# Performance work log

Hardware: AMD Instinct MI355X
Metric: run time of the kernel (lower is better)

The kernel has to match this reference:

```python
import jax, jax.numpy as jnp
import numpy as np

B, T, D = 2048, 200, 256

def setup_inputs() -> dict:
    key = jax.random.key(0)
    k1, k2, k3, k4, k5 = jax.random.split(key, 5)
    query = jax.random.normal(k1, (B, 1, D), dtype=jnp.float32)
    user_behavior = jax.random.normal(k2, (B, T, D), dtype=jnp.float32)
    mask = jax.random.bernoulli(k3, 0.5, (B, T))
    # nn.Linear weights: linear1 (2D -> D), linear2 (D -> 1), no bias
    W1 = jax.random.normal(k4, (D, 2 * D), dtype=jnp.float32) * (1.0 / np.sqrt(2 * D))
    W2 = jax.random.normal(k5, (1, D), dtype=jnp.float32) * (1.0 / np.sqrt(D))
    return {"query": query, "user_behavior": user_behavior, "mask": mask, "W1": W1, "W2": W2}

def reference(query, user_behavior, mask, W1, W2):
    T_ = user_behavior.shape[1]
    queries = jnp.broadcast_to(query, (query.shape[0], T_, query.shape[2]))  # [B,T,D]
    attn_in = jnp.concatenate([queries, user_behavior], axis=-1)  # [B,T,2D]
    h = jnp.tanh(jnp.einsum('btk,dk->btd', attn_in, W1))          # [B,T,D]
    score = jnp.einsum('btd,od->bot', h, W2)                       # [B,1,T] (transpose(1,2) of [B,T,1])
    # masked_fill with 0 BEFORE softmax, as in the original module
    score = jnp.where(mask[:, None, :], jnp.zeros((), score.dtype), score)
    attn = jax.nn.softmax(score, axis=-1)                          # [B,1,T]
    out = jnp.matmul(attn, user_behavior)                          # [B,1,D]
    return jnp.squeeze(out)                                        # [B,D]
```

## Files before the change

### kernel.cpp

```cpp
#include <hip/hip_runtime.h>
#include <hip/hip_bf16.h>

typedef __bf16 bf16_t;
typedef __bf16 bf16x8 __attribute__((ext_vector_type(8)));
typedef float  f32x4  __attribute__((ext_vector_type(4)));

#define T_LEN 200
#define D_DIM 256
#define NTILE 13
#define NB    2

__device__ __forceinline__ float fast_tanh(float x) {
    float e = __expf(2.0f * x);
    return 1.0f - 2.0f / (e + 1.0f);
}

__global__ __launch_bounds__(256) void qpart_kernel(
    const float* __restrict__ Q, const float* __restrict__ W1,
    float* __restrict__ Out)
{
    __shared__ float qs[8][256];
    const int tid = threadIdx.x;
    const int b0  = blockIdx.x * 8;
    for (int idx = tid; idx < 8 * 256; idx += 256)
        qs[idx >> 8][idx & 255] = Q[(size_t)(b0 + (idx >> 8)) * 256 + (idx & 255)];
    __syncthreads();
    float acc[8];
    #pragma unroll
    for (int i = 0; i < 8; ++i) acc[i] = 0.f;
    const f32x4* Wv = (const f32x4*)(W1 + (size_t)tid * 512);
    #pragma unroll 4
    for (int k4 = 0; k4 < 64; ++k4) {
        f32x4 w = Wv[k4];
        #pragma unroll
        for (int bb = 0; bb < 8; ++bb) {
            f32x4 qv = *(const f32x4*)&qs[bb][k4 * 4];
            acc[bb] += qv[0]*w[0] + qv[1]*w[1] + qv[2]*w[2] + qv[3]*w[3];
        }
    }
    #pragma unroll
    for (int bb = 0; bb < 8; ++bb)
        Out[(size_t)(b0 + bb) * 256 + tid] = acc[bb];
}

__global__ __launch_bounds__(512, 4) void attn_main_kernel(
    const float* __restrict__ U,
    const int*   __restrict__ Mask,
    const float* __restrict__ W1,
    const float* __restrict__ W2,
    float* __restrict__ Out)
{
    __shared__ bf16_t ubt[3][16 * 256];
    __shared__ float score_lds[NTILE][16];
    __shared__ int   msk_lds[208];
    __shared__ float out_lds[4][256];
    __shared__ float l_lds[4];

    const int tid  = threadIdx.x;
    const int lane = tid & 63;
    const int wv   = tid >> 6;
    const int lr   = lane & 15;
    const int lg   = lane >> 4;

    bf16x8 bq[2][8];
    float  w2v[2];
    #pragma unroll
    for (int n = 0; n < 2; ++n) {
        const int d = wv * 32 + n * 16 + lr;
        const float* wrow = W1 + (size_t)d * 512 + 256;
        #pragma unroll
        for (int kk = 0; kk < 8; ++kk) {
            const float* s = wrow + kk * 32 + lg * 8;
            f32x4 lo = *(const f32x4*)s;
            f32x4 hi = *(const f32x4*)(s + 4);
            bf16x8 v;
            v[0]=(bf16_t)lo[0]; v[1]=(bf16_t)lo[1]; v[2]=(bf16_t)lo[2]; v[3]=(bf16_t)lo[3];
            v[4]=(bf16_t)hi[0]; v[5]=(bf16_t)hi[1]; v[6]=(bf16_t)hi[2]; v[7]=(bf16_t)hi[3];
            bq[n][kk] = v;
        }
        w2v[n] = W2[d];
    }

    const int srow = tid >> 5;
    const int scol = (tid & 31) * 8;
    const unsigned swoff = (unsigned)srow * 512
                         + (((unsigned)scol * 2) ^ (((unsigned)srow & 7) << 4));
    const int dp = tid & 127;
    const int jg = tid >> 7;

    for (int bb = 0; bb < NB; ++bb) {
        const int b = blockIdx.x * NB + bb;
        const float* Ub = U + (size_t)b * (T_LEN * D_DIM);

        float qp[2];
        #pragma unroll
        for (int n = 0; n < 2; ++n)
            qp[n] = Out[(size_t)b * 256 + wv * 32 + n * 16 + lr];

        for (int idx = tid; idx < NTILE * 16; idx += 512)
            ((float*)score_lds)[idx] = 0.f;
        if (tid < 208)
            msk_lds[tid] = (tid < T_LEN) ? Mask[(size_t)b * T_LEN + tid] : 1;

        float op0 = 0.f, op1 = 0.f, l_part = 0.f;

        {
            const float* src = Ub + (size_t)srow * 256 + scol;
            f32x4 g0 = *(const f32x4*)src;
            f32x4 g1 = *(const f32x4*)(src + 4);
            bf16x8 v;
            v[0]=(bf16_t)g0[0]; v[1]=(bf16_t)g0[1]; v[2]=(bf16_t)g0[2]; v[3]=(bf16_t)g0[3];
            v[4]=(bf16_t)g1[0]; v[5]=(bf16_t)g1[1]; v[6]=(bf16_t)g1[2]; v[7]=(bf16_t)g1[3];
            *(bf16x8*)((char*)&ubt[0][0] + swoff) = v;
        }
        __syncthreads();

        for (int it = 0; it < NTILE; ++it) {
            char* const bcur = (char*)&ubt[it % 3][0];
            char* const bnxt = (char*)&ubt[(it + 1) % 3][0];

            f32x4 g0 = {0.f,0.f,0.f,0.f}, g1 = {0.f,0.f,0.f,0.f};
            bool stage_w = false;
            if (it + 1 < NTILE) {
                const int t = (it + 1) * 16 + srow;
                if (t < T_LEN) {
                    const float* src = Ub + (size_t)t * 256 + scol;
                    g0 = *(const f32x4*)src;
                    g1 = *(const f32x4*)(src + 4);
                    stage_w = true;
                }
            }

            f32x4 acc0 = {0.f,0.f,0.f,0.f}, acc1 = {0.f,0.f,0.f,0.f};
            #pragma unroll
            for (int kk = 0; kk < 8; ++kk) {
                const unsigned kb   = (unsigned)(kk * 64 + lg * 16);
                const unsigned aoff = (unsigned)lr * 512
                                    + (kb ^ (((unsigned)lr & 7) << 4));
                bf16x8 a = *(const bf16x8*)(bcur + aoff);
                acc0 = __builtin_amdgcn_mfma_f32_16x16x32_bf16(a, bq[0][kk], acc0, 0, 0, 0);
                acc1 = __builtin_amdgcn_mfma_f32_16x16x32_bf16(a, bq[1][kk], acc1, 0, 0, 0);
            }

            if (stage_w) {
                bf16x8 v;
                v[0]=(bf16_t)g0[0]; v[1]=(bf16_t)g0[1]; v[2]=(bf16_t)g0[2]; v[3]=(bf16_t)g0[3];
                v[4]=(bf16_t)g1[0]; v[5]=(bf16_t)g1[1]; v[6]=(bf16_t)g1[2]; v[7]=(bf16_t)g1[3];
                *(bf16x8*)(bnxt + swoff) = v;
            }

            float sp[4];
            #pragma unroll
            for (int r = 0; r < 4; ++r) {
                float h0 = fast_tanh(acc0[r] + qp[0]);
                float h1 = fast_tanh(acc1[r] + qp[1]);
                sp[r] = h0 * w2v[0] + h1 * w2v[1];
            }
            #pragma unroll
            for (int r = 0; r < 4; ++r) {
                sp[r] += __shfl_xor(sp[r], 1);
                sp[r] += __shfl_xor(sp[r], 2);
                sp[r] += __shfl_xor(sp[r], 4);
                sp[r] += __shfl_xor(sp[r], 8);
            }
            if (lr == 0) {
                #pragma unroll
                for (int r = 0; r < 4; ++r)
                    atomicAdd(&score_lds[it][lg * 4 + r], sp[r]);
            }

            __syncthreads();

            #pragma unroll
            for (int jj = 0; jj < 4; ++jj) {
                const int j = jg * 4 + jj;
                const int t = it * 16 + j;
                const float s = score_lds[it][j];
                float p = 0.f;
                if (t < T_LEN)
                    p = msk_lds[t] ? 1.0f : __expf(s);
                l_part += p;
                const unsigned off = (unsigned)j * 512
                                   + (((unsigned)dp * 4) ^ (((unsigned)j & 7) << 4));
                const unsigned w = *(const unsigned*)(bcur + off);
                const float u0 = __builtin_bit_cast(float, w << 16);
                const float u1 = __builtin_bit_cast(float, w & 0xffff0000u);
                op0 += p * u0;
                op1 += p * u1;
            }
        }

        out_lds[jg][dp * 2]     = op0;
        out_lds[jg][dp * 2 + 1] = op1;
        if ((tid & 127) == 0) l_lds[jg] = l_part;
        __syncthreads();
        if (tid < 256) {
            const float l = l_lds[0] + l_lds[1] + l_lds[2] + l_lds[3];
            const float o = out_lds[0][tid] + out_lds[1][tid]
                          + out_lds[2][tid] + out_lds[3][tid];
            Out[(size_t)b * 256 + tid] = o / l;
        }
        __syncthreads();
    }
}

extern "C" void kernel_launch(void* const* d_in, const int* in_sizes, int n_in,
                              void* d_out, int out_size, void* d_ws, size_t ws_size,
                              hipStream_t stream)
{
    const float* Q  = (const float*)d_in[0];
    const float* U  = (const float*)d_in[1];
    const int*   Mk = (const int*)d_in[2];
    const float* W1 = (const float*)d_in[3];
    const float* W2 = (const float*)d_in[4];
    float* Out = (float*)d_out;
    const int B = in_sizes[0] / D_DIM;

    qpart_kernel<<<dim3(B / 8), dim3(256), 0, stream>>>(Q, W1, Out);
    attn_main_kernel<<<dim3(B / NB), dim3(512), 0, stream>>>(U, Mk, W1, W2, Out);
}
```

Baseline: 207.3 us.

## Use one batch row per block and do the weighted sum after scoring

Each block now handles a single batch row instead of two, which doubles the grid. The per-tile weighted sum over bf16 LDS tiles is removed. Scores are accumulated for all tiles first, then softmax weights are computed once into LDS, and a final pass re-reads U from global memory in fp32 to form the output. This shortens the per-tile critical path and gives fp32 accuracy in the output sum, at the cost of a second read of each U row (likely served from L2) and a larger grid that reloads W1 fragments per row.

```diff
diff --git a/kernel.cpp b/kernel.cpp
--- a/kernel.cpp
+++ b/kernel.cpp
@@ -8,7 +8,6 @@
 #define T_LEN 200
 #define D_DIM 256
 #define NTILE 13
-#define NB    2
 
 __device__ __forceinline__ float fast_tanh(float x) {
     float e = __expf(2.0f * x);
@@ -51,16 +50,17 @@
     float* __restrict__ Out)
 {
     __shared__ bf16_t ubt[3][16 * 256];
-    __shared__ float score_lds[NTILE][16];
-    __shared__ int   msk_lds[208];
+    __shared__ float score_lds[208];
+    __shared__ float p_lds[208];
     __shared__ float out_lds[4][256];
-    __shared__ float l_lds[4];
+    __shared__ float l_lds;
 
     const int tid  = threadIdx.x;
     const int lane = tid & 63;
     const int wv   = tid >> 6;
     const int lr   = lane & 15;
     const int lg   = lane >> 4;
+    const int b    = blockIdx.x;
 
     bf16x8 bq[2][8];
     float  w2v[2];
@@ -81,126 +81,126 @@
         w2v[n] = W2[d];
     }
 
+    const float* Ub = U + (size_t)b * (T_LEN * D_DIM);
+
+    float qp[2];
+    #pragma unroll
+    for (int n = 0; n < 2; ++n)
+        qp[n] = Out[(size_t)b * 256 + wv * 32 + n * 16 + lr];
+
+    if (tid < 208) score_lds[tid] = 0.f;
+    if (tid == 0)  l_lds = 0.f;
+
     const int srow = tid >> 5;
     const int scol = (tid & 31) * 8;
     const unsigned swoff = (unsigned)srow * 512
                          + (((unsigned)scol * 2) ^ (((unsigned)srow & 7) << 4));
-    const int dp = tid & 127;
-    const int jg = tid >> 7;
-
-    for (int bb = 0; bb < NB; ++bb) {
-        const int b = blockIdx.x * NB + bb;
-        const float* Ub = U + (size_t)b * (T_LEN * D_DIM);
-
-        float qp[2];
-        #pragma unroll
-        for (int n = 0; n < 2; ++n)
-            qp[n] = Out[(size_t)b * 256 + wv * 32 + n * 16 + lr];
-
-        for (int idx = tid; idx < NTILE * 16; idx += 512)
-            ((float*)score_lds)[idx] = 0.f;
-        if (tid < 208)
-            msk_lds[tid] = (tid < T_LEN) ? Mask[(size_t)b * T_LEN + tid] : 1;
-
-        float op0 = 0.f, op1 = 0.f, l_part = 0.f;
-
-        {
-            const float* src = Ub + (size_t)srow * 256 + scol;
-            f32x4 g0 = *(const f32x4*)src;
-            f32x4 g1 = *(const f32x4*)(src + 4);
+
+    {
+        const float* src = Ub + (size_t)srow * 256 + scol;
+        f32x4 g0 = *(const f32x4*)src;
+        f32x4 g1 = *(const f32x4*)(src + 4);
+        bf16x8 v;
+        v[0]=(bf16_t)g0[0]; v[1]=(bf16_t)g0[1]; v[2]=(bf16_t)g0[2]; v[3]=(bf16_t)g0[3];
+        v[4]=(bf16_t)g1[0]; v[5]=(bf16_t)g1[1]; v[6]=(bf16_t)g1[2]; v[7]=(bf16_t)g1[3];
+        *(bf16x8*)((char*)&ubt[0][0] + swoff) = v;
+    }
+    __syncthreads();
+
+    for (int it = 0; it < NTILE; ++it) {
+        char* const bcur = (char*)&ubt[it % 3][0];
+        char* const bnxt = (char*)&ubt[(it + 1) % 3][0];
+
+        f32x4 g0 = {0.f,0.f,0.f,0.f}, g1 = {0.f,0.f,0.f,0.f};
+        bool stage_w = false;
+        if (it + 1 < NTILE) {
+            const int t = (it + 1) * 16 + srow;
+            if (t < T_LEN) {
+                const float* src = Ub + (size_t)t * 256 + scol;
+                g0 = *(const f32x4*)src;
+                g1 = *(const f32x4*)(src + 4);
+                stage_w = true;
+            }
+        }
+
+        f32x4 acc0 = {0.f,0.f,0.f,0.f}, acc1 = {0.f,0.f,0.f,0.f};
+        #pragma unroll
+        for (int kk = 0; kk < 8; ++kk) {
+            const unsigned kb   = (unsigned)(kk * 64 + lg * 16);
+            const unsigned aoff = (unsigned)lr * 512
+                                + (kb ^ (((unsigned)lr & 7) << 4));
+            bf16x8 a = *(const bf16x8*)(bcur + aoff);
+            acc0 = __builtin_amdgcn_mfma_f32_16x16x32_bf16(a, bq[0][kk], acc0, 0, 0, 0);
+            acc1 = __builtin_amdgcn_mfma_f32_16x16x32_bf16(a, bq[1][kk], acc1, 0, 0, 0);
+        }
+
+        if (stage_w) {
             bf16x8 v;
             v[0]=(bf16_t)g0[0]; v[1]=(bf16_t)g0[1]; v[2]=(bf16_t)g0[2]; v[3]=(bf16_t)g0[3];
             v[4]=(bf16_t)g1[0]; v[5]=(bf16_t)g1[1]; v[6]=(bf16_t)g1[2]; v[7]=(bf16_t)g1[3];
-            *(bf16x8*)((char*)&ubt[0][0] + swoff) = v;
-        }
+            *(bf16x8*)(bnxt + swoff) = v;
+        }
+
+        float sp[4];
+        #pragma unroll
+        for (int r = 0; r < 4; ++r) {
+            float h0 = fast_tanh(acc0[r] + qp[0]);
+            float h1 = fast_tanh(acc1[r] + qp[1]);
+            sp[r] = h0 * w2v[0] + h1 * w2v[1];
+        }
+        #pragma unroll
+        for (int r = 0; r < 4; ++r) {
+            sp[r] += __shfl_xor(sp[r], 1);
+            sp[r] += __shfl_xor(sp[r], 2);
+            sp[r] += __shfl_xor(sp[r], 4);
+            sp[r] += __shfl_xor(sp[r], 8);
+        }
+        if (lr == 0) {
+            #pragma unroll
+            for (int r = 0; r < 4; ++r)
+                atomicAdd(&score_lds[it * 16 + lg * 4 + r], sp[r]);
+        }
+
         __syncthreads();
-
-        for (int it = 0; it < NTILE; ++it) {
-            char* const bcur = (char*)&ubt[it % 3][0];
-            char* const bnxt = (char*)&ubt[(it + 1) % 3][0];
-
-            f32x4 g0 = {0.f,0.f,0.f,0.f}, g1 = {0.f,0.f,0.f,0.f};
-            bool stage_w = false;
-            if (it + 1 < NTILE) {
-                const int t = (it + 1) * 16 + srow;
-                if (t < T_LEN) {
-                    const float* src = Ub + (size_t)t * 256 + scol;
-                    g0 = *(const f32x4*)src;
-                    g1 = *(const f32x4*)(src + 4);
-                    stage_w = true;
-                }
-            }
-
-            f32x4 acc0 = {0.f,0.f,0.f,0.f}, acc1 = {0.f,0.f,0.f,0.f};
-            #pragma unroll
-            for (int kk = 0; kk < 8; ++kk) {
-                const unsigned kb   = (unsigned)(kk * 64 + lg * 16);
-                const unsigned aoff = (unsigned)lr * 512
-                                    + (kb ^ (((unsigned)lr & 7) << 4));
-                bf16x8 a = *(const bf16x8*)(bcur + aoff);
-                acc0 = __builtin_amdgcn_mfma_f32_16x16x32_bf16(a, bq[0][kk], acc0, 0, 0, 0);
-                acc1 = __builtin_amdgcn_mfma_f32_16x16x32_bf16(a, bq[1][kk], acc1, 0, 0, 0);
-            }
-
-            if (stage_w) {
-                bf16x8 v;
-                v[0]=(bf16_t)g0[0]; v[1]=(bf16_t)g0[1]; v[2]=(bf16_t)g0[2]; v[3]=(bf16_t)g0[3];
-                v[4]=(bf16_t)g1[0]; v[5]=(bf16_t)g1[1]; v[6]=(bf16_t)g1[2]; v[7]=(bf16_t)g1[3];
-                *(bf16x8*)(bnxt + swoff) = v;
-            }
-
-            float sp[4];
-            #pragma unroll
-            for (int r = 0; r < 4; ++r) {
-                float h0 = fast_tanh(acc0[r] + qp[0]);
-                float h1 = fast_tanh(acc1[r] + qp[1]);
-                sp[r] = h0 * w2v[0] + h1 * w2v[1];
-            }
-            #pragma unroll
-            for (int r = 0; r < 4; ++r) {
-                sp[r] += __shfl_xor(sp[r], 1);
-                sp[r] += __shfl_xor(sp[r], 2);
-                sp[r] += __shfl_xor(sp[r], 4);
-                sp[r] += __shfl_xor(sp[r], 8);
-            }
-            if (lr == 0) {
-                #pragma unroll
-                for (int r = 0; r < 4; ++r)
-                    atomicAdd(&score_lds[it][lg * 4 + r], sp[r]);
-            }
-
-            __syncthreads();
-
-            #pragma unroll
-            for (int jj = 0; jj < 4; ++jj) {
-                const int j = jg * 4 + jj;
-                const int t = it * 16 + j;
-                const float s = score_lds[it][j];
-                float p = 0.f;
-                if (t < T_LEN)
-                    p = msk_lds[t] ? 1.0f : __expf(s);
-                l_part += p;
-                const unsigned off = (unsigned)j * 512
-                                   + (((unsigned)dp * 4) ^ (((unsigned)j & 7) << 4));
-                const unsigned w = *(const unsigned*)(bcur + off);
-                const float u0 = __builtin_bit_cast(float, w << 16);
-                const float u1 = __builtin_bit_cast(float, w & 0xffff0000u);
-                op0 += p * u0;
-                op1 += p * u1;
-            }
-        }
-
-        out_lds[jg][dp * 2]     = op0;
-        out_lds[jg][dp * 2 + 1] = op1;
-        if ((tid & 127) == 0) l_lds[jg] = l_part;
-        __syncthreads();
-        if (tid < 256) {
-            const float l = l_lds[0] + l_lds[1] + l_lds[2] + l_lds[3];
-            const float o = out_lds[0][tid] + out_lds[1][tid]
-                          + out_lds[2][tid] + out_lds[3][tid];
-            Out[(size_t)b * 256 + tid] = o / l;
-        }
-        __syncthreads();
+    }
+
+    {
+        float p = 0.f;
+        if (tid < T_LEN)
+            p = Mask[(size_t)b * T_LEN + tid] ? 1.0f : __expf(score_lds[tid]);
+        if (tid < 208) p_lds[tid] = p;
+        float ps = p;
+        ps += __shfl_xor(ps, 1);
+        ps += __shfl_xor(ps, 2);
+        ps += __shfl_xor(ps, 4);
+        ps += __shfl_xor(ps, 8);
+        ps += __shfl_xor(ps, 16);
+        ps += __shfl_xor(ps, 32);
+        if (lane == 0 && ps != 0.f) atomicAdd(&l_lds, ps);
+    }
+    __syncthreads();
+
+    {
+        const int dp = tid & 127;
+        const int jg = tid >> 7;
+        float o0 = 0.f, o1 = 0.f;
+        const float* Up = Ub + (size_t)(jg * 50) * 256 + dp * 2;
+        #pragma unroll 5
+        for (int i = 0; i < 50; ++i) {
+            const float p = p_lds[jg * 50 + i];
+            const float2 u = *(const float2*)(Up + (size_t)i * 256);
+            o0 += p * u.x;
+            o1 += p * u.y;
+        }
+        out_lds[jg][dp * 2]     = o0;
+        out_lds[jg][dp * 2 + 1] = o1;
+    }
+    __syncthreads();
+
+    if (tid < 256) {
+        const float o = out_lds[0][tid] + out_lds[1][tid]
+                      + out_lds[2][tid] + out_lds[3][tid];
+        Out[(size_t)b * 256 + tid] = o / l_lds;
     }
 }
 
@@ -217,5 +217,5 @@
     const int B = in_sizes[0] / D_DIM;
 
     qpart_kernel<<<dim3(B / 8), dim3(256), 0, stream>>>(Q, W1, Out);
-    attn_main_kernel<<<dim3(B / NB), dim3(512), 0, stream>>>(U, Mk, W1, W2, Out);
-}
+    attn_main_kernel<<<dim3(B), dim3(512), 0, stream>>>(U, Mk, W1, W2, Out);
+}
```

Measured after the change: 225.1 us. +8.6%, slower.
